# Kernel tuning notes

Measured on AMD Instinct MI355X. Metric: run time of the kernel, lower is better.

## Reference

```python
import jax, jax.numpy as jnp
import numpy as np

D_MODEL = 1024
N_HEADS = 16


def setup_inputs() -> dict:
    key = jax.random.key(0)
    ks = jax.random.split(key, 5)
    sigma = (1.0 / D_MODEL) ** 0.5
    return {
        "x": jax.random.normal(ks[0], (4, 2048, D_MODEL), dtype=jnp.float32),
        "W_q": jax.random.normal(ks[1], (D_MODEL, D_MODEL), dtype=jnp.float32) * sigma,
        "W_k": jax.random.normal(ks[2], (D_MODEL, D_MODEL), dtype=jnp.float32) * sigma,
        "W_v": jax.random.normal(ks[3], (D_MODEL, D_MODEL), dtype=jnp.float32) * sigma,
        "W_o": jax.random.normal(ks[4], (D_MODEL, D_MODEL), dtype=jnp.float32) * sigma,
    }


def reference(x, W_q, W_k, W_v, W_o):
    b, s, d = x.shape
    h = N_HEADS
    d_h = d // h
    # Projections: original does einsum('d_out dim, ... dim -> ... d_out') == x @ W.T
    def proj(W):
        y = jnp.einsum('bsd,ed->bse', x, W)
        # ... seq (head d_h) -> ... head seq d_h
        return y.reshape(b, s, h, d_h).transpose(0, 2, 1, 3)
    Q, K, V = proj(W_q), proj(W_k), proj(W_v)
    scale = 1.0 / jnp.sqrt(jnp.asarray(d_h, dtype=x.dtype))
    scores = jnp.einsum('bhqd,bhkd->bhqk', Q, K) * scale  # [b,h,s,s]
    causal = jnp.tril(jnp.ones((s, s), dtype=bool))
    scores = jnp.where(causal, scores, -jnp.inf)
    attn = jax.nn.softmax(scores, axis=-1)
    out = jnp.einsum('bhqk,bhkd->bhqd', attn, V)  # [b,h,s,d_h]
    out = out.transpose(0, 2, 1, 3).reshape(b, s, d)
    # einsum(Temp, W_o, '... dim1, dim dim1 -> ... dim') == Temp @ W_o.T
    return jnp.einsum('bse,de->bsd', out, W_o)
```

## Files before the change

### kernel.cpp

```cpp
#include <hip/hip_runtime.h>

typedef __attribute__((ext_vector_type(8))) short s16x8;
typedef __attribute__((ext_vector_type(4))) float f32x4;
typedef unsigned short u16;
typedef unsigned int u32;
typedef unsigned long long u64;

__device__ __forceinline__ u16 f2bf(float f) {
  unsigned u = __builtin_bit_cast(unsigned, f);
  return (u16)((u + 0x7fffu + ((u >> 16) & 1u)) >> 16);
}

#define QSCALE 0.18033688011112042f
#define MFIX 16.0f

__device__ __forceinline__ void gld16(const u16* g, u16* l) {
  __builtin_amdgcn_global_load_lds(
      (const __attribute__((address_space(1))) void*)g,
      (__attribute__((address_space(3))) void*)l, 16, 0, 0);
}

__device__ __forceinline__ u32 pack_trunc(float a, float b) {
  return __builtin_amdgcn_perm(__builtin_bit_cast(u32, b),
                               __builtin_bit_cast(u32, a), 0x07060302u);
}

__global__ __launch_bounds__(256)
void cvt_bf16(const float* __restrict__ src, u16* __restrict__ dst, int n8)
{
  const int i = blockIdx.x * 256 + threadIdx.x;
  if (i < n8) {
    f32x4 a = ((const f32x4*)src)[2 * i];
    f32x4 b = ((const f32x4*)src)[2 * i + 1];
    s16x8 pk;
    pk[0] = (short)f2bf(a[0]); pk[1] = (short)f2bf(a[1]);
    pk[2] = (short)f2bf(a[2]); pk[3] = (short)f2bf(a[3]);
    pk[4] = (short)f2bf(b[0]); pk[5] = (short)f2bf(b[1]);
    pk[6] = (short)f2bf(b[2]); pk[7] = (short)f2bf(b[3]);
    ((s16x8*)dst)[i] = pk;
  }
}

__global__ __launch_bounds__(256)
void cvt_bf16_w(const float* __restrict__ s0, const float* __restrict__ s1,
                const float* __restrict__ s2, const float* __restrict__ s3,
                u16* __restrict__ d0, u16* __restrict__ d1,
                u16* __restrict__ d2, u16* __restrict__ d3)
{
  const int ws = blockIdx.y;
  const float* src = (ws == 0) ? s0 : (ws == 1) ? s1 : (ws == 2) ? s2 : s3;
  u16* dst = (ws == 0) ? d0 : (ws == 1) ? d1 : (ws == 2) ? d2 : d3;
  const int i = blockIdx.x * 256 + threadIdx.x;
  f32x4 a = ((const f32x4*)src)[2 * i];
  f32x4 b = ((const f32x4*)src)[2 * i + 1];
  s16x8 pk;
  pk[0] = (short)f2bf(a[0]); pk[1] = (short)f2bf(a[1]);
  pk[2] = (short)f2bf(a[2]); pk[3] = (short)f2bf(a[3]);
  pk[4] = (short)f2bf(b[0]); pk[5] = (short)f2bf(b[1]);
  pk[6] = (short)f2bf(b[2]); pk[7] = (short)f2bf(b[3]);
  ((s16x8*)dst)[i] = pk;
}

template<bool OUT_QKV>
__global__ __launch_bounds__(256)
void gemm97(const u16* __restrict__ A,
            const u16* __restrict__ B0, const u16* __restrict__ B1,
            const u16* __restrict__ B2,
            u16* __restrict__ o0, u16* __restrict__ o1, u16* __restrict__ o2,
            float* __restrict__ oF)
{
  const int by = blockIdx.x;
  const int bx = blockIdx.y;
  const int bz = blockIdx.z;
  const u16* B = (bz == 0) ? B0 : ((bz == 1) ? B1 : B2);
  u16* oQ = (bz == 0) ? o0 : ((bz == 1) ? o1 : o2);

  __shared__ u16 As[128 * 32];
  __shared__ u16 Bs[128 * 32];

  const int tid  = threadIdx.x;
  const int w    = tid >> 6;
  const int lane = tid & 63;
  const int quad = lane >> 4;
  const int l15  = lane & 15;
  const int wm   = (w >> 1) * 64;
  const int wn   = (w & 1) * 64;

  const int arb  = w * 32;
  const int srow = lane >> 2;
  const int scol = (lane & 3) * 8;
  const u16* ga = A + (size_t)(by * 128 + arb + srow) * 1024 + scol;
  const u16* gb = B + (size_t)(bx * 128 + arb + srow) * 1024 + scol;
  u16* la0 = &As[arb * 32];
  u16* la1 = &As[(arb + 16) * 32];
  u16* lb0 = &Bs[arb * 32];
  u16* lb1 = &Bs[(arb + 16) * 32];

  f32x4 acc[4][4];
  #pragma unroll
  for (int i = 0; i < 4; ++i)
    #pragma unroll
    for (int j = 0; j < 4; ++j)
      acc[i][j] = (f32x4){0.f, 0.f, 0.f, 0.f};

  for (int k0 = 0; k0 < 1024; k0 += 32) {
    gld16(ga + k0,               la0);
    gld16(ga + k0 + 16 * 1024,   la1);
    gld16(gb + k0,               lb0);
    gld16(gb + k0 + 16 * 1024,   lb1);
    __syncthreads();

    s16x8 af[4], bf[4];
    #pragma unroll
    for (int i = 0; i < 4; ++i)
      af[i] = *(const s16x8*)&As[(wm + i * 16 + l15) * 32 + quad * 8];
    #pragma unroll
    for (int i = 0; i < 4; ++i)
      bf[i] = *(const s16x8*)&Bs[(wn + i * 16 + l15) * 32 + quad * 8];
    #pragma unroll
    for (int mt = 0; mt < 4; ++mt)
      #pragma unroll
      for (int nt = 0; nt < 4; ++nt)
        acc[mt][nt] = __builtin_amdgcn_mfma_f32_16x16x32_bf16(
            af[mt], bf[nt], acc[mt][nt], 0, 0, 0);
    __syncthreads();
  }

  #pragma unroll
  for (int mt = 0; mt < 4; ++mt)
    #pragma unroll
    for (int nt = 0; nt < 4; ++nt)
      #pragma unroll
      for (int r = 0; r < 4; ++r) {
        const int row = by * 128 + wm + mt * 16 + quad * 4 + r;
        const int col = bx * 128 + wn + nt * 16 + l15;
        float v = acc[mt][nt][r];
        if (OUT_QKV) {
          if (bz == 0) v *= QSCALE;
          const int b = row >> 11, s = row & 2047, hh = col >> 6, d = col & 63;
          oQ[(size_t)(b * 16 + hh) * 131072 + s * 64 + d] = f2bf(v);
        } else {
          oF[(size_t)row * 1024 + col] = v;
        }
      }
}

__global__ __launch_bounds__(256)
void vtrans(const u16* __restrict__ Vb, u16* __restrict__ VT)
{
  const int st = blockIdx.x;
  const int bh = blockIdx.y;
  __shared__ u16 T[64 * 72];
  const int tid = threadIdx.x;
  const size_t base = (size_t)bh * 131072;
  #pragma unroll
  for (int p = 0; p < 2; ++p) {
    const int idx = tid + p * 256;
    const int row = idx >> 3;
    const int col = (idx & 7) * 8;
    s16x8 v = *(const s16x8*)(Vb + base + (size_t)(st * 64 + row) * 64 + col);
    #pragma unroll
    for (int e = 0; e < 8; ++e) T[(col + e) * 72 + row] = v[e];
  }
  __syncthreads();
  #pragma unroll
  for (int p = 0; p < 2; ++p) {
    const int idx = tid + p * 256;
    const int drow = idx >> 3;
    const int scol = (idx & 7) * 8;
    *(s16x8*)(VT + base + (size_t)drow * 2048 + st * 64 + scol) =
        *(const s16x8*)&T[drow * 72 + scol];
  }
}

#define LOADKV(jj)                                                             \
  do {                                                                         \
    _Pragma("unroll")                                                          \
    for (int p = 0; p < 2; ++p) {                                              \
      const int idx = tid + p * 256;                                           \
      const int key = idx >> 3, col = (idx & 7) * 8;                           \
      kreg[p] = *(const s16x8*)(Kg + base + (size_t)((jj) * 64 + key) * 64 + col); \
    }                                                                          \
    _Pragma("unroll")                                                          \
    for (int p = 0; p < 2; ++p) {                                              \
      const int idx = tid + p * 256;                                           \
      const int d = idx >> 3, col = (idx & 7) * 8;                             \
      vreg[p] = *(const s16x8*)(VTg + base + (size_t)d * 2048 + (jj) * 64 + col); \
    }                                                                          \
  } while (0)

#define STOREKV()                                                              \
  do {                                                                         \
    _Pragma("unroll")                                                          \
    for (int p = 0; p < 2; ++p) {                                              \
      const int idx = tid + p * 256;                                           \
      const int key = idx >> 3, col = (idx & 7) * 8;                           \
      const int slot = (key & 3) * 16 + (key >> 2);                            \
      *(s16x8*)&Ks[slot * 72 + col] = kreg[p];                                 \
    }                                                                          \
    _Pragma("unroll")                                                          \
    for (int p = 0; p < 2; ++p) {                                              \
      const int idx = tid + p * 256;                                           \
      const int d = idx >> 3, col = (idx & 7) * 8;                             \
      *(s16x8*)&Vt[d * 72 + col] = vreg[p];                                    \
    }                                                                          \
  } while (0)

__global__ __launch_bounds__(256, 5)
void attn_kernel(const u16* __restrict__ Qg, const u16* __restrict__ Kg,
                 const u16* __restrict__ VTg, u16* __restrict__ out)
{
  const int bh = blockIdx.x;
  const int qt = 31 - blockIdx.y;
  const int b = bh >> 4, h = bh & 15;

  __shared__ u16 Ks[64 * 72];
  __shared__ u16 Vt[64 * 72];
  __shared__ u16 Ps[64 * 72];

  const int tid = threadIdx.x;
  const int w = tid >> 6, lane = tid & 63, quad = lane >> 4, l15 = lane & 15;
  const size_t base = (size_t)bh * 131072;

  s16x8 aq[2];
  #pragma unroll
  for (int ks = 0; ks < 2; ++ks)
    aq[ks] = *(const s16x8*)(Qg + base +
        (size_t)(qt * 64 + w * 16 + l15) * 64 + ks * 32 + quad * 8);

  u16* Pw = &Ps[(w * 16) * 72];

  s16x8 ones;
  #pragma unroll
  for (int e = 0; e < 8; ++e) ones[e] = (short)0x3F80;

  f32x4 O[4], liacc;
  #pragma unroll
  for (int dt = 0; dt < 4; ++dt) O[dt] = (f32x4){0.f, 0.f, 0.f, 0.f};
  liacc = (f32x4){0.f, 0.f, 0.f, 0.f};

  s16x8 kreg[2], vreg[2];
  LOADKV(0);
  STOREKV();
  __syncthreads();

  for (int j = 0; j <= qt; ++j) {
    if (j < qt) LOADKV(j + 1);

    f32x4 S[4];
    __builtin_amdgcn_s_setprio(1);
    #pragma unroll
    for (int nt = 0; nt < 4; ++nt) {
      s16x8 b0 = *(const s16x8*)&Ks[(nt * 16 + l15) * 72 + quad * 8];
      s16x8 b1 = *(const s16x8*)&Ks[(nt * 16 + l15) * 72 + 32 + quad * 8];
      f32x4 z = (f32x4){-MFIX, -MFIX, -MFIX, -MFIX};
      z = __builtin_amdgcn_mfma_f32_16x16x32_bf16(aq[0], b0, z, 0, 0, 0);
      z = __builtin_amdgcn_mfma_f32_16x16x32_bf16(aq[1], b1, z, 0, 0, 0);
      S[nt] = z;
    }
    __builtin_amdgcn_s_setprio(0);

    if (j == qt) {
      #pragma unroll
      for (int nt = 0; nt < 4; ++nt)
        #pragma unroll
        for (int r = 0; r < 4; ++r) {
          const int kg = 4 * l15 + nt;
          const int qg = w * 16 + quad * 4 + r;
          if (kg > qg) S[nt][r] = -1e30f;
        }
    }

    #pragma unroll
    for (int r = 0; r < 4; ++r) {
      const float p0 = __builtin_amdgcn_exp2f(S[0][r]);
      const float p1 = __builtin_amdgcn_exp2f(S[1][r]);
      const float p2 = __builtin_amdgcn_exp2f(S[2][r]);
      const float p3 = __builtin_amdgcn_exp2f(S[3][r]);
      const u64 pk = (u64)pack_trunc(p0, p1) |
                     ((u64)pack_trunc(p2, p3) << 32);
      *(u64*)&Pw[(quad * 4 + r) * 72 + 4 * l15] = pk;
    }
    s16x8 a0 = *(const s16x8*)&Pw[l15 * 72 + quad * 8];
    s16x8 a1 = *(const s16x8*)&Pw[l15 * 72 + 32 + quad * 8];

    __builtin_amdgcn_s_setprio(1);
    liacc = __builtin_amdgcn_mfma_f32_16x16x32_bf16(a0, ones, liacc, 0, 0, 0);
    liacc = __builtin_amdgcn_mfma_f32_16x16x32_bf16(a1, ones, liacc, 0, 0, 0);
    #pragma unroll
    for (int dt = 0; dt < 4; ++dt) {
      s16x8 b0 = *(const s16x8*)&Vt[(dt * 16 + l15) * 72 + quad * 8];
      s16x8 b1 = *(const s16x8*)&Vt[(dt * 16 + l15) * 72 + 32 + quad * 8];
      O[dt] = __builtin_amdgcn_mfma_f32_16x16x32_bf16(a0, b0, O[dt], 0, 0, 0);
      O[dt] = __builtin_amdgcn_mfma_f32_16x16x32_bf16(a1, b1, O[dt], 0, 0, 0);
    }
    __builtin_amdgcn_s_setprio(0);

    __syncthreads();
    if (j < qt) {
      STOREKV();
      __syncthreads();
    }
  }

  #pragma unroll
  for (int r = 0; r < 4; ++r) {
    const float inv = __builtin_amdgcn_rcpf(liacc[r]);
    const int sq = qt * 64 + w * 16 + quad * 4 + r;
    #pragma unroll
    for (int dt = 0; dt < 4; ++dt)
      out[(size_t)(b * 2048 + sq) * 1024 + h * 64 + dt * 16 + l15] =
          f2bf(O[dt][r] * inv);
  }
}

extern "C" void kernel_launch(void* const* d_in, const int* in_sizes, int n_in,
                              void* d_out, int out_size, void* d_ws, size_t ws_size,
                              hipStream_t stream) {
  (void)in_sizes; (void)n_in; (void)out_size; (void)ws_size;
  const float* x  = (const float*)d_in[0];
  const float* Wq = (const float*)d_in[1];
  const float* Wk = (const float*)d_in[2];
  const float* Wv = (const float*)d_in[3];
  const float* Wo = (const float*)d_in[4];
  float* out = (float*)d_out;

  u16* W16 = (u16*)d_ws;
  u16* xb  = W16;
  u16* VT  = W16;
  u16* Qb  = W16 + 8388608;
  u16* Kb  = W16 + 16777216;
  u16* Vb  = W16 + 25165824;
  u16* AO  = Vb;
  u16* Wqb = W16 + 33554432;
  u16* Wkb = Wqb + 1048576;
  u16* Wvb = Wkb + 1048576;
  u16* Wob = Wvb + 1048576;

  dim3 blk(256);
  cvt_bf16<<<dim3(4096), blk, 0, stream>>>(x,  xb,  1048576);
  cvt_bf16_w<<<dim3(512, 4), blk, 0, stream>>>(Wq, Wk, Wv, Wo,
                                               Wqb, Wkb, Wvb, Wob);

  gemm97<true ><<<dim3(64, 8, 3), blk, 0, stream>>>(
      xb, Wqb, Wkb, Wvb, Qb, Kb, Vb, nullptr);
  vtrans<<<dim3(32, 64), blk, 0, stream>>>(Vb, VT);
  attn_kernel<<<dim3(64, 32), blk, 0, stream>>>(Qb, Kb, VT, AO);
  gemm97<false><<<dim3(64, 8, 1), blk, 0, stream>>>(
      AO, Wob, Wob, Wob, nullptr, nullptr, nullptr, out);
}
```

Before: 251.0 us.

## Replace QKV projection GEMM with 256x256-tile double-buffered swizzled kernel

Adds a dedicated QKV projection kernel that uses 512 threads, 256x256 output tiles and K-steps of 64. Two LDS buffers are filled with global_load_lds, the LDS columns are XOR-swizzled to avoid bank conflicts, and waitcnt/barriers are set by hand so the next tile loads while MFMAs run. The goal is more operand reuse per byte loaded and less load latency exposed in the largest GEMM. The cost is much higher LDS (64KB) and register use, only 384 blocks, and hand-written sync that is easy to get wrong. The output-projection GEMM is split into its own non-templated kernel and is otherwise unchanged.

Measured after the change: 259.3 us. 3.3% more time.

```diff
diff --git a/kernel.cpp b/kernel.cpp
--- a/kernel.cpp
+++ b/kernel.cpp
@@ -61,19 +61,122 @@
   ((s16x8*)dst)[i] = pk;
 }
 
-template<bool OUT_QKV>
-__global__ __launch_bounds__(256)
-void gemm97(const u16* __restrict__ A,
-            const u16* __restrict__ B0, const u16* __restrict__ B1,
-            const u16* __restrict__ B2,
-            u16* __restrict__ o0, u16* __restrict__ o1, u16* __restrict__ o2,
-            float* __restrict__ oF)
+__global__ __launch_bounds__(512)
+void gemmQKV(const u16* __restrict__ A,
+             const u16* __restrict__ B0, const u16* __restrict__ B1,
+             const u16* __restrict__ B2,
+             u16* __restrict__ o0, u16* __restrict__ o1, u16* __restrict__ o2)
 {
   const int by = blockIdx.x;
   const int bx = blockIdx.y;
-  const int bz = blockIdx.z;
-  const u16* B = (bz == 0) ? B0 : ((bz == 1) ? B1 : B2);
+  const int bz = bx >> 2;
+  const u16* Bw = (bz == 0) ? B0 : ((bz == 1) ? B1 : B2);
   u16* oQ = (bz == 0) ? o0 : ((bz == 1) ? o1 : o2);
+
+  __shared__ u16 As[2][256 * 64];
+  __shared__ u16 Bs[2][256 * 64];
+
+  const int tid  = threadIdx.x;
+  const int wid  = tid >> 6;
+  const int lane = tid & 63;
+  const int quad = lane >> 4;
+  const int l15  = lane & 15;
+  const int wr   = wid >> 2;
+  const int wc   = wid & 3;
+
+  const int srow = tid >> 3;
+  const int scol = ((tid & 7) ^ (srow & 7)) * 8;
+  const int wb8  = wid * 8;
+  const u16* Ag = A  + (size_t)(by * 256) * 1024;
+  const u16* Bg = Bw + (size_t)((bx & 3) * 256) * 1024;
+
+#define STAGE(bf, kt)                                                          \
+  do {                                                                         \
+    _Pragma("unroll")                                                          \
+    for (int c = 0; c < 4; ++c) {                                              \
+      gld16(Ag + (size_t)(c * 64 + srow) * 1024 + (kt) * 64 + scol,            \
+            &As[bf][(c * 64 + wb8) * 64]);                                     \
+      gld16(Bg + (size_t)(c * 64 + srow) * 1024 + (kt) * 64 + scol,            \
+            &Bs[bf][(c * 64 + wb8) * 64]);                                     \
+    }                                                                          \
+  } while (0)
+
+  f32x4 acc[8][4];
+  #pragma unroll
+  for (int i = 0; i < 8; ++i)
+    #pragma unroll
+    for (int j = 0; j < 4; ++j)
+      acc[i][j] = (f32x4){0.f, 0.f, 0.f, 0.f};
+
+  const int swz = (l15 & 7) * 8;
+  const int ca0 = (quad * 8) ^ swz;
+  const int ca1 = (32 + quad * 8) ^ swz;
+
+  STAGE(0, 0);
+  STAGE(1, 1);
+  asm volatile("s_waitcnt vmcnt(8)" ::: "memory");
+  __builtin_amdgcn_s_barrier();
+  __builtin_amdgcn_sched_barrier(0);
+
+  for (int kt = 0; kt < 16; ++kt) {
+    const int bf = kt & 1;
+    const u16* Ab = &As[bf][(wr * 128) * 64];
+    const u16* Bb = &Bs[bf][(wc * 64) * 64];
+    __builtin_amdgcn_s_setprio(1);
+    #pragma unroll
+    for (int kh = 0; kh < 2; ++kh) {
+      const int cc = kh ? ca1 : ca0;
+      s16x8 bfr[4];
+      #pragma unroll
+      for (int nt = 0; nt < 4; ++nt)
+        bfr[nt] = *(const s16x8*)&Bb[(nt * 16 + l15) * 64 + cc];
+      #pragma unroll
+      for (int mt = 0; mt < 8; ++mt) {
+        s16x8 af = *(const s16x8*)&Ab[(mt * 16 + l15) * 64 + cc];
+        #pragma unroll
+        for (int nt = 0; nt < 4; ++nt)
+          acc[mt][nt] = __builtin_amdgcn_mfma_f32_16x16x32_bf16(
+              af, bfr[nt], acc[mt][nt], 0, 0, 0);
+      }
+    }
+    __builtin_amdgcn_s_setprio(0);
+    if (kt == 15) break;
+    asm volatile("s_waitcnt lgkmcnt(0)" ::: "memory");
+    __builtin_amdgcn_sched_barrier(0);
+    __builtin_amdgcn_s_barrier();
+    if (kt < 14) {
+      STAGE(bf, kt + 2);
+      asm volatile("s_waitcnt vmcnt(8)" ::: "memory");
+    } else {
+      asm volatile("s_waitcnt vmcnt(0)" ::: "memory");
+    }
+    __builtin_amdgcn_sched_barrier(0);
+    __builtin_amdgcn_s_barrier();
+    __builtin_amdgcn_sched_barrier(0);
+  }
+
+  #pragma unroll
+  for (int mt = 0; mt < 8; ++mt)
+    #pragma unroll
+    for (int nt = 0; nt < 4; ++nt)
+      #pragma unroll
+      for (int r = 0; r < 4; ++r) {
+        const int row = by * 256 + wr * 128 + mt * 16 + quad * 4 + r;
+        const int col = (bx & 3) * 256 + wc * 64 + nt * 16 + l15;
+        float v = acc[mt][nt][r];
+        if (bz == 0) v *= QSCALE;
+        const int b = row >> 11, s = row & 2047, hh = col >> 6, d = col & 63;
+        oQ[(size_t)(b * 16 + hh) * 131072 + s * 64 + d] = f2bf(v);
+      }
+#undef STAGE
+}
+
+__global__ __launch_bounds__(256)
+void gemm97o(const u16* __restrict__ A, const u16* __restrict__ B,
+             float* __restrict__ oF)
+{
+  const int by = blockIdx.x;
+  const int bx = blockIdx.y;
 
   __shared__ u16 As[128 * 32];
   __shared__ u16 Bs[128 * 32];
@@ -134,14 +237,7 @@
       for (int r = 0; r < 4; ++r) {
         const int row = by * 128 + wm + mt * 16 + quad * 4 + r;
         const int col = bx * 128 + wn + nt * 16 + l15;
-        float v = acc[mt][nt][r];
-        if (OUT_QKV) {
-          if (bz == 0) v *= QSCALE;
-          const int b = row >> 11, s = row & 2047, hh = col >> 6, d = col & 63;
-          oQ[(size_t)(b * 16 + hh) * 131072 + s * 64 + d] = f2bf(v);
-        } else {
-          oF[(size_t)row * 1024 + col] = v;
-        }
+        oF[(size_t)row * 1024 + col] = acc[mt][nt][r];
       }
 }
 
@@ -342,10 +438,9 @@
   cvt_bf16_w<<<dim3(512, 4), blk, 0, stream>>>(Wq, Wk, Wv, Wo,
                                                Wqb, Wkb, Wvb, Wob);
 
-  gemm97<true ><<<dim3(64, 8, 3), blk, 0, stream>>>(
-      xb, Wqb, Wkb, Wvb, Qb, Kb, Vb, nullptr);
+  gemmQKV<<<dim3(32, 12), dim3(512), 0, stream>>>(
+      xb, Wqb, Wkb, Wvb, Qb, Kb, Vb);
   vtrans<<<dim3(32, 64), blk, 0, stream>>>(Vb, VT);
   attn_kernel<<<dim3(64, 32), blk, 0, stream>>>(Qb, Kb, VT, AO);
-  gemm97<false><<<dim3(64, 8, 1), blk, 0, stream>>>(
-      AO, Wob, Wob, Wob, nullptr, nullptr, nullptr, out);
-}
+  gemm97o<<<dim3(64, 8), blk, 0, stream>>>(AO, Wob, out);
+}
```
